# Optimization experiments

Hardware: AMD Instinct MI355X
Metric: run time of the kernel (lower is better)

The kernel has to match this reference:

```python
import jax, jax.numpy as jnp
from jax import lax
import numpy as np

B, T, F_IN, H = 64, 128, 12, 128  # batch, seq_len, input/output features, hidden


def _uinit(key, shape, fan):
    return jax.random.uniform(key, shape, jnp.float32, -1.0, 1.0) / np.float32(np.sqrt(fan))


def setup_inputs() -> dict:
    key = jax.random.key(0)
    ks = jax.random.split(key, 12)
    inp = {
        "x": jax.random.normal(ks[0], (B, T, F_IN), jnp.float32),
        # encoder LSTM (gate order i,f,g,o; b = b_ih + b_hh folded together)
        "enc_Wih": _uinit(ks[1], (4 * H, F_IN), H),
        "enc_Whh": _uinit(ks[2], (4 * H, H), H),
        "enc_b": _uinit(ks[3], (4 * H,), H),
        # decoder LSTM (input is the 12-dim teacher-forced x slice)
        "dec_Wih": _uinit(ks[4], (4 * H, F_IN), H),
        "dec_Whh": _uinit(ks[5], (4 * H, H), H),
        "dec_b": _uinit(ks[6], (4 * H,), H),
        # attention: Linear(2H -> H) with bias, then v: Linear(H -> 1, no bias)
        "attn_W": _uinit(ks[7], (H, 2 * H), 2 * H),
        "attn_b": _uinit(ks[8], (H,), 2 * H),
        "v_w": _uinit(ks[9], (H,), H),
        # output layer: Linear(2H -> F_IN)  (intended width; see notes)
        "out_W": _uinit(ks[10], (F_IN, 2 * H), 2 * H),
        "out_b": _uinit(ks[11], (F_IN,), 2 * H),
    }
    return inp


def _lstm_cell(xt, h, c, Wih, Whh, b):
    z = xt @ Wih.T + h @ Whh.T + b  # [B, 4H]
    i, f, g, o = jnp.split(z, 4, axis=-1)
    c = jax.nn.sigmoid(f) * c + jax.nn.sigmoid(i) * jnp.tanh(g)
    h = jax.nn.sigmoid(o) * jnp.tanh(c)
    return h, c


def reference(x, enc_Wih, enc_Whh, enc_b, dec_Wih, dec_Whh, dec_b,
              attn_W, attn_b, v_w, out_W, out_b):
    b_, t_, _ = x.shape
    hdim = enc_Whh.shape[1]
    xs = jnp.swapaxes(x, 0, 1)  # [T, B, F]
    h0 = jnp.zeros((b_, hdim), x.dtype)
    c0 = jnp.zeros((b_, hdim), x.dtype)

    def enc_step(carry, xt):
        h, c = carry
        h, c = _lstm_cell(xt, h, c, enc_Wih, enc_Whh, enc_b)
        return (h, c), h

    (hT, cT), enc_hs = lax.scan(enc_step, (h0, c0), xs)
    enc_out = jnp.swapaxes(enc_hs, 0, 1)  # [B, T, H]

    # split attn weight: cat(hidden, enc_out) @ W.T == hidden@W1.T + enc_out@W2.T
    W1, W2 = attn_W[:, :hdim], attn_W[:, hdim:]
    enc_proj = jnp.einsum("bth,gh->btg", enc_out, W2)  # precompute encoder side

    def dec_step(carry, xt):
        h, c = carry
        h, c = _lstm_cell(xt, h, c, dec_Wih, dec_Whh, dec_b)
        energy = jnp.tanh((h @ W1.T)[:, None, :] + enc_proj + attn_b)  # [B,T,H]
        score = jnp.einsum("bth,h->bt", energy, v_w)
        w = jax.nn.softmax(score, axis=1)  # attention over encoder time
        ctx = jnp.einsum("bt,bth->bh", w, enc_out)
        return (h, c), jnp.concatenate([h, ctx], axis=-1)  # [B, 2H]

    _, dec_ys = lax.scan(dec_step, (hT, cT), xs)
    dec_out = jnp.swapaxes(dec_ys, 0, 1)  # [B, T, 2H]
    return dec_out @ out_W.T + out_b  # [B, T, F]
```

## Files before the change

### kernel.cpp

```cpp
#include <hip/hip_runtime.h>
#include <hip/hip_bf16.h>

#define BB 64
#define TT 128
#define FIN 12
#define HH 128

#define LOG2E 1.4426950408889634f
#define TWO_LOG2E 2.8853900817779268f

__device__ __forceinline__ float fexp2(float x) { return __builtin_amdgcn_exp2f(x); }
__device__ __forceinline__ float frcp(float x)  { return __builtin_amdgcn_rcpf(x); }

__device__ __forceinline__ float tanh_f(float x) {
  return 1.0f - 2.0f * frcp(1.0f + fexp2(TWO_LOG2E * x));
}
__device__ __forceinline__ float sigm_f(float x) {
  return frcp(1.0f + fexp2(-LOG2E * x));
}

template <int CTRL>
__device__ __forceinline__ float dpp_addstage(float v) {
  int s = __builtin_amdgcn_update_dpp(0, __float_as_int(v), CTRL, 0xF, 0xF, true);
  return v + __int_as_float(s);
}
__device__ __forceinline__ float red8(float v) {
  v = dpp_addstage<0xB1>(v);
  v = dpp_addstage<0x4E>(v);
  v = dpp_addstage<0x141>(v);
  return v;
}

#define FMA4S(acc, s, v) do { \
  acc.x = fmaf((s), (v).x, acc.x); \
  acc.y = fmaf((s), (v).y, acc.y); \
  acc.z = fmaf((s), (v).z, acc.z); \
  acc.w = fmaf((s), (v).w, acc.w); } while (0)

#define ACC4(hv, wv, a) do { \
  a = fmaf((hv).x, (wv).x, a); a = fmaf((hv).y, (wv).y, a); \
  a = fmaf((hv).z, (wv).z, a); a = fmaf((hv).w, (wv).w, a); } while (0)

__device__ __forceinline__ void lstm_phase(
    const float* __restrict__ Wih, const float* __restrict__ Whh,
    const float* __restrict__ bias, float* __restrict__ Hout ,
    float* __restrict__ xs, float (*hbuf)[160], float* __restrict__ hist,
    const int tid, const int q, const int i, float& c)
{
  const int xo   = (q < 4) ? 3 * q : 0;
  const float xz = (q < 4) ? 1.0f : 0.0f;

  float4 wg[4][4];
  #pragma unroll
  for (int g = 0; g < 4; ++g)
    #pragma unroll
    for (int j = 0; j < 4; ++j)
      wg[g][j] = *(const float4*)(Whh + ((g * HH + i) * HH) + 16 * q + 4 * j);

  float wx[4][3];
  #pragma unroll
  for (int g = 0; g < 4; ++g)
    #pragma unroll
    for (int j = 0; j < 3; ++j)
      wx[g][j] = Wih[(g * HH + i) * FIN + xo + j] * xz;

  const float bi = bias[i], bf = bias[HH + i], bg = bias[2 * HH + i], bo = bias[3 * HH + i];

  int ts = 0;
  #pragma unroll 1
  for (int half = 0; half < 2; ++half) {
    #pragma unroll 1
    for (int tt = 0; tt < 64; ++tt, ++ts) {
      const int t = half * 64 + tt;
      __syncthreads();
      const float* hb = (const float*)hbuf[ts & 1] + q * 20;
      float4 h0 = *(const float4*)(hb + 0);
      float4 h1 = *(const float4*)(hb + 4);
      float4 h2 = *(const float4*)(hb + 8);
      float4 h3 = *(const float4*)(hb + 12);

      const float* xt = xs + t * FIN + xo;
      float x0 = xt[0], x1 = xt[1], x2 = xt[2];
      float ai = wx[0][0] * x0 + wx[0][1] * x1 + wx[0][2] * x2;
      float af = wx[1][0] * x0 + wx[1][1] * x1 + wx[1][2] * x2;
      float ag = wx[2][0] * x0 + wx[2][1] * x1 + wx[2][2] * x2;
      float ao = wx[3][0] * x0 + wx[3][1] * x1 + wx[3][2] * x2;

      ACC4(h0, wg[0][0], ai); ACC4(h0, wg[1][0], af); ACC4(h0, wg[2][0], ag); ACC4(h0, wg[3][0], ao);
      ACC4(h1, wg[0][1], ai); ACC4(h1, wg[1][1], af); ACC4(h1, wg[2][1], ag); ACC4(h1, wg[3][1], ao);
      ACC4(h2, wg[0][2], ai); ACC4(h2, wg[1][2], af); ACC4(h2, wg[2][2], ag); ACC4(h2, wg[3][2], ao);
      ACC4(h3, wg[0][3], ai); ACC4(h3, wg[1][3], af); ACC4(h3, wg[2][3], ag); ACC4(h3, wg[3][3], ao);

      ai = red8(ai); af = red8(af); ag = red8(ag); ao = red8(ao);

      if (q == 0) {
        float zi = sigm_f(ai + bi);
        float zf = sigm_f(af + bf);
        float zg = tanh_f(ag + bg);
        float zo = sigm_f(ao + bo);
        c = fmaf(zf, c, zi * zg);
        float hn = zo * tanh_f(c);
        hbuf[(ts + 1) & 1][(i >> 4) * 20 + (i & 15)] = hn;
        hist[tt * HH + i] = hn;
      }
    }
    __syncthreads();
    {
      float4* dst = (float4*)(Hout + (size_t)(half * 64) * HH);
      const float4* src = (const float4*)hist;
      dst[tid]        = src[tid];
      dst[tid + 1024] = src[tid + 1024];
    }
  }
}

__global__ __launch_bounds__(1024, 4) void lstm_enc_kernel(
    const float* __restrict__ x,
    const float* __restrict__ eWih, const float* __restrict__ eWhh, const float* __restrict__ eb,
    float* __restrict__ encH, float* __restrict__ decH)
{
  const int b   = blockIdx.x;
  const int tid = threadIdx.x;
  const int q   = tid & 7;
  const int i   = tid >> 3;

  __shared__ __align__(16) float xs[TT * FIN];
  __shared__ __align__(16) float hbuf[2][160];
  __shared__ __align__(16) float hist[64 * HH];

  if (tid < (TT * FIN / 4))
    ((float4*)xs)[tid] = ((const float4*)(x + (size_t)b * TT * FIN))[tid];
  if (tid < 320) ((float*)hbuf)[tid] = 0.0f;
  float c = 0.0f;

  lstm_phase(eWih, eWhh, eb, encH + (size_t)b * TT * HH, xs, hbuf, hist, tid, q, i, c);

  if (q == 0) decH[(size_t)b * TT * HH + i] = c;
}

__global__ __launch_bounds__(1024, 4) void lstm_dec_p_kernel(
    const float* __restrict__ x,
    const float* __restrict__ dWih, const float* __restrict__ dWhh, const float* __restrict__ db,
    const float* __restrict__ attnW, const float* __restrict__ outW,
    const float* __restrict__ encH,
    float* __restrict__ decH, float* __restrict__ Pbuf, float* __restrict__ y2buf)
{
  __shared__ __align__(16) float smem[12416];
  const int tid = threadIdx.x;

  if (blockIdx.x < 64) {
    const int b = blockIdx.x;
    const int q = tid & 7;
    const int i = tid >> 3;
    float* xs           = smem;
    float (*hbuf)[160]  = (float(*)[160])(smem + 1536);
    float* hist         = smem + 1856;

    if (tid < (TT * FIN / 4))
      ((float4*)xs)[tid] = ((const float4*)(x + (size_t)b * TT * FIN))[tid];
    if (tid < 128) {
      float hv = encH[((size_t)b * TT + 127) * HH + tid];
      hbuf[0][(tid >> 4) * 20 + (tid & 15)] = hv;
    }
    float c = 0.0f;
    if (q == 0) c = decH[(size_t)b * TT * HH + i];

    lstm_phase(dWih, dWhh, db, decH + (size_t)b * TT * HH, xs, hbuf, hist, tid, q, i, c);
  } else if (blockIdx.x < 192) {
    const int pb = blockIdx.x - 64;
    const int b  = pb & 63;
    const int r0 = (pb >> 6) * 64;
    float* WT = smem;
    float* Xt = smem + 4224;

    const float* X = encH + ((size_t)b * TT + r0) * HH;
    ((float4*)Xt)[tid]        = ((const float4*)X)[tid];
    ((float4*)Xt)[tid + 1024] = ((const float4*)X)[tid + 1024];

    const float* W = attnW + HH;
    const int hq = tid & 31, rr = tid >> 5;
    const int h0 = 4 * hq;

    float4 acc0 = make_float4(0.f, 0.f, 0.f, 0.f);
    float4 acc1 = acc0;

    #pragma unroll 1
    for (int kb = 0; kb < 4; ++kb) {
      __syncthreads();
      {
        int h = tid >> 3, koff = (tid & 7) * 4;
        float4 v = *(const float4*)(W + h * 256 + kb * 32 + koff);
        WT[(koff + 0) * 132 + h] = v.x;
        WT[(koff + 1) * 132 + h] = v.y;
        WT[(koff + 2) * 132 + h] = v.z;
        WT[(koff + 3) * 132 + h] = v.w;
      }
      __syncthreads();
      const float* xr0 = Xt + (2 * rr) * 128 + kb * 32;
      const float* xr1 = xr0 + 128;
      #pragma unroll
      for (int k4 = 0; k4 < 32; k4 += 4) {
        float4 xa = *(const float4*)(xr0 + k4);
        float4 xb = *(const float4*)(xr1 + k4);
        float4 w0 = *(const float4*)&WT[(k4 + 0) * 132 + h0];
        float4 w1 = *(const float4*)&WT[(k4 + 1) * 132 + h0];
        float4 w2 = *(const float4*)&WT[(k4 + 2) * 132 + h0];
        float4 w3 = *(const float4*)&WT[(k4 + 3) * 132 + h0];
        FMA4S(acc0, xa.x, w0); FMA4S(acc0, xa.y, w1);
        FMA4S(acc0, xa.z, w2); FMA4S(acc0, xa.w, w3);
        FMA4S(acc1, xb.x, w0); FMA4S(acc1, xb.y, w1);
        FMA4S(acc1, xb.z, w2); FMA4S(acc1, xb.w, w3);
      }
    }
    acc0.x = fexp2(TWO_LOG2E * acc0.x); acc0.y = fexp2(TWO_LOG2E * acc0.y);
    acc0.z = fexp2(TWO_LOG2E * acc0.z); acc0.w = fexp2(TWO_LOG2E * acc0.w);
    acc1.x = fexp2(TWO_LOG2E * acc1.x); acc1.y = fexp2(TWO_LOG2E * acc1.y);
    acc1.z = fexp2(TWO_LOG2E * acc1.z); acc1.w = fexp2(TWO_LOG2E * acc1.w);
    float* O = Pbuf + ((size_t)b * TT + r0) * HH;
    *(float4*)(O + (2 * rr) * 128 + h0)     = acc0;
    *(float4*)(O + (2 * rr + 1) * 128 + h0) = acc1;
  } else if (y2buf) {
    const int b = blockIdx.x - 192;
    float* w2l = smem;
    if (tid < 384) {
      int f = tid >> 5, k = (tid & 31) * 4;
      float4 wv = *(const float4*)(outW + f * 256 + 128 + k);
      *(float4*)&w2l[f * 132 + k] = wv;
    }
    __syncthreads();
    for (int j = tid; j < TT * 12; j += 1024) {
      int t = j / 12, f = j - 12 * t;
      const float* er = encH + ((size_t)b * TT + t) * HH;
      const float* wr = w2l + f * 132;
      float a = 0.f;
      #pragma unroll 8
      for (int k = 0; k < 32; ++k) {
        float4 ev = *(const float4*)(er + 4 * k);
        float4 wv = *(const float4*)(wr + 4 * k);
        ACC4(ev, wv, a);
      }
      y2buf[b * (TT * 16) + t * 16 + f] = a;
    }
  }
}

__global__ __launch_bounds__(256, 2) void projA_kernel(
    const float* __restrict__ decH, const float* __restrict__ attnW,
    const float* __restrict__ attnb, float* __restrict__ Abuf)
{
  const int b  = blockIdx.x & 63;
  const int r0 = (blockIdx.x >> 6) * 16;
  const int tid = threadIdx.x;

  __shared__ __align__(16) float WT[64 * 128];
  __shared__ __align__(16) float Xt[16 * 128];

  const float* X = decH + ((size_t)b * TT + r0) * HH;
  const float* W = attnW;

  ((float4*)Xt)[tid]       = ((const float4*)X)[tid];
  ((float4*)Xt)[256 + tid] = ((const float4*)X)[256 + tid];

  const int hq = tid & 31, rr = tid >> 5;
  const int h0 = 4 * hq;

  float4 acc0 = *(const float4*)(attnb + h0);
  float4 acc1 = acc0;

  for (int kb = 0; kb < 2; ++kb) {
    __syncthreads();
    {
      int h = tid >> 1, koff = (tid & 1) * 32;
      #pragma unroll
      for (int j = 0; j < 8; ++j) {
        float4 v = *(const float4*)(W + h * 256 + kb * 64 + koff + 4 * j);
        int kp = koff + 4 * j;
        WT[(kp + 0) * 128 + h] = v.x;
        WT[(kp + 1) * 128 + h] = v.y;
        WT[(kp + 2) * 128 + h] = v.z;
        WT[(kp + 3) * 128 + h] = v.w;
      }
    }
    __syncthreads();
    const float* xr0 = Xt + (2 * rr) * 128 + kb * 64;
    const float* xr1 = xr0 + 128;
    #pragma unroll
    for (int k4 = 0; k4 < 64; k4 += 4) {
      float4 xa = *(const float4*)(xr0 + k4);
      float4 xb = *(const float4*)(xr1 + k4);
      float4 w0 = *(const float4*)&WT[(k4 + 0) * 128 + h0];
      float4 w1 = *(const float4*)&WT[(k4 + 1) * 128 + h0];
      float4 w2 = *(const float4*)&WT[(k4 + 2) * 128 + h0];
      float4 w3 = *(const float4*)&WT[(k4 + 3) * 128 + h0];
      FMA4S(acc0, xa.x, w0); FMA4S(acc0, xa.y, w1);
      FMA4S(acc0, xa.z, w2); FMA4S(acc0, xa.w, w3);
      FMA4S(acc1, xb.x, w0); FMA4S(acc1, xb.y, w1);
      FMA4S(acc1, xb.z, w2); FMA4S(acc1, xb.w, w3);
    }
  }
  acc0.x = fexp2(TWO_LOG2E * acc0.x); acc0.y = fexp2(TWO_LOG2E * acc0.y);
  acc0.z = fexp2(TWO_LOG2E * acc0.z); acc0.w = fexp2(TWO_LOG2E * acc0.w);
  acc1.x = fexp2(TWO_LOG2E * acc1.x); acc1.y = fexp2(TWO_LOG2E * acc1.y);
  acc1.z = fexp2(TWO_LOG2E * acc1.z); acc1.w = fexp2(TWO_LOG2E * acc1.w);
  float* O = Abuf + ((size_t)b * TT + r0) * HH;
  *(float4*)(O + (2 * rr) * 128 + h0)     = acc0;
  *(float4*)(O + (2 * rr + 1) * 128 + h0) = acc1;
}

#define AST 132
#define Y2ST 20

template <bool HY2>
__global__ __launch_bounds__(512, 2) void attn_kernel(
    const float* __restrict__ encH, const float* __restrict__ decH,
    const float* __restrict__ Pbuf, const float* __restrict__ Abuf,
    const float* __restrict__ y2buf,
    const float* __restrict__ vw, const float* __restrict__ outW,
    const float* __restrict__ outb, float* __restrict__ out)
{
  const int b  = blockIdx.x >> 3;
  const int s0 = (blockIdx.x & 7) * 16;
  const int tid = threadIdx.x;

  __shared__ __align__(16) float buf[64 * 128];
  __shared__ __align__(16) float a_lds[16 * AST];
  __shared__ __align__(16) float sc[16 * AST];
  __shared__ __align__(16) float dh[16 * 128];
  __shared__ __align__(16) float vl[HH];
  __shared__ __align__(16) float y2s[TT * Y2ST];
  __shared__ __align__(16) float w2l[12 * AST];

  ((float4*)dh)[tid] = ((const float4*)(decH + ((size_t)b * TT + s0) * HH))[tid];
  if (tid < 32) ((float4*)vl)[tid] = ((const float4*)vw)[tid];
  {
    int r = tid >> 5, c4 = (tid & 31) * 4;
    float4 av = *(const float4*)(Abuf + ((size_t)b * TT + s0 + r) * HH + c4);
    *(float4*)&a_lds[r * AST + c4] = av;
  }
  if constexpr (HY2) {
    if (tid < 512) {
      float4 v = ((const float4*)(y2buf + (size_t)b * (TT * 16)))[tid];
      int t = tid >> 2, g = (tid & 3) * 4;
      *(float4*)&y2s[t * Y2ST + g] = v;
    }
  } else {
    if (tid < 384) {
      int f = tid >> 5, k = (tid & 31) * 4;
      float4 wv = *(const float4*)(outW + f * 256 + 128 + k);
      *(float4*)&w2l[f * AST + k] = wv;
    }
  }

  const int u  = tid & 31;
  const int sl = tid >> 5;
  const int uq = u & 15;
  const int uh = u >> 4;

  for (int half = 0; half < 2; ++half) {
    const int tbase = half * 64;
    __syncthreads();
    #pragma unroll
    for (int i = 0; i < 4; ++i) {
      int flat = i * 2048 + tid * 4;
      int tp = flat >> 7;
      int h0 = flat & 127;
      float4 v = *(const float4*)(Pbuf + ((size_t)b * TT + tbase + tp) * HH + h0);
      int tq = tp >> 2, tr = tp & 3;
      buf[(h0 + 0) * 64 + 4 * ((tq ^ ((h0 + 0) >> 2)) & 15) + tr] = v.x;
      buf[(h0 + 1) * 64 + 4 * ((tq ^ ((h0 + 1) >> 2)) & 15) + tr] = v.y;
      buf[(h0 + 2) * 64 + 4 * ((tq ^ ((h0 + 2) >> 2)) & 15) + tr] = v.z;
      buf[(h0 + 3) * 64 + 4 * ((tq ^ ((h0 + 3) >> 2)) & 15) + tr] = v.w;
    }
    __syncthreads();
    float4 acc = make_float4(0.f, 0.f, 0.f, 0.f);
    const float* earow = a_lds + sl * AST;
    #pragma unroll 4
    for (int hh = 0; hh < 64; hh += 4) {
      const int h = uh * 64 + hh;
      float4 ea = *(const float4*)&earow[h];
      float4 va = *(const float4*)&vl[h];
      const int xoff = 4 * ((uq ^ ((h >> 2) & 15)) & 15);
      float4 p0 = *(const float4*)&buf[(h + 0) * 64 + xoff];
      float4 p1 = *(const float4*)&buf[(h + 1) * 64 + xoff];
      float4 p2 = *(const float4*)&buf[(h + 2) * 64 + xoff];
      float4 p3 = *(const float4*)&buf[(h + 3) * 64 + xoff];
      acc.x = fmaf(va.x, frcp(fmaf(ea.x, p0.x, 1.f)), acc.x);
      acc.y = fmaf(va.x, frcp(fmaf(ea.x, p0.y, 1.f)), acc.y);
      acc.z = fmaf(va.x, frcp(fmaf(ea.x, p0.z, 1.f)), acc.z);
      acc.w = fmaf(va.x, frcp(fmaf(ea.x, p0.w, 1.f)), acc.w);
      acc.x = fmaf(va.y, frcp(fmaf(ea.y, p1.x, 1.f)), acc.x);
      acc.y = fmaf(va.y, frcp(fmaf(ea.y, p1.y, 1.f)), acc.y);
      acc.z = fmaf(va.y, frcp(fmaf(ea.y, p1.z, 1.f)), acc.z);
      acc.w = fmaf(va.y, frcp(fmaf(ea.y, p1.w, 1.f)), acc.w);
      acc.x = fmaf(va.z, frcp(fmaf(ea.z, p2.x, 1.f)), acc.x);
      acc.y = fmaf(va.z, frcp(fmaf(ea.z, p2.y, 1.f)), acc.y);
      acc.z = fmaf(va.z, frcp(fmaf(ea.z, p2.z, 1.f)), acc.z);
      acc.w = fmaf(va.z, frcp(fmaf(ea.z, p2.w, 1.f)), acc.w);
      acc.x = fmaf(va.w, frcp(fmaf(ea.w, p3.x, 1.f)), acc.x);
      acc.y = fmaf(va.w, frcp(fmaf(ea.w, p3.y, 1.f)), acc.y);
      acc.z = fmaf(va.w, frcp(fmaf(ea.w, p3.z, 1.f)), acc.z);
      acc.w = fmaf(va.w, frcp(fmaf(ea.w, p3.w, 1.f)), acc.w);
    }
    acc.x += __shfl_xor(acc.x, 16, 64);
    acc.y += __shfl_xor(acc.y, 16, 64);
    acc.z += __shfl_xor(acc.z, 16, 64);
    acc.w += __shfl_xor(acc.w, 16, 64);
    if (uh == 0) {
      float4 o;
      o.x = -2.f * acc.x; o.y = -2.f * acc.y;
      o.z = -2.f * acc.z; o.w = -2.f * acc.w;
      *(float4*)&sc[sl * AST + tbase + 4 * uq] = o;
    }
  }
  __syncthreads();

  {
    float4 sv = *(const float4*)&sc[sl * AST + 4 * u];
    float mx = fmaxf(fmaxf(sv.x, sv.y), fmaxf(sv.z, sv.w));
    #pragma unroll
    for (int msk = 1; msk <= 16; msk <<= 1) mx = fmaxf(mx, __shfl_xor(mx, msk, 64));
    float4 e;
    e.x = fexp2(LOG2E * (sv.x - mx));
    e.y = fexp2(LOG2E * (sv.y - mx));
    e.z = fexp2(LOG2E * (sv.z - mx));
    e.w = fexp2(LOG2E * (sv.w - mx));
    float sm = (e.x + e.y) + (e.z + e.w);
    #pragma unroll
    for (int msk = 1; msk <= 16; msk <<= 1) sm += __shfl_xor(sm, msk, 64);
    float r = frcp(sm);
    e.x *= r; e.y *= r; e.z *= r; e.w *= r;
    *(float4*)&sc[sl * AST + 4 * u] = e;
  }

  if constexpr (!HY2) {
    for (int half = 0; half < 2; ++half) {
      const int tbase = half * 64;
      __syncthreads();
      #pragma unroll
      for (int i = 0; i < 4; ++i) {
        int flat = i * 2048 + tid * 4;
        int tp = flat >> 7;
        int hh0 = flat & 127;
        *(float4*)&buf[tp * 128 + hh0] =
            *(const float4*)(encH + ((size_t)b * TT + tbase + tp) * HH + hh0);
      }
      __syncthreads();
      {
        int j = tid;
        int t = j / 12, f = j - 12 * t;
        float a = 0.f;
        const float* br = buf + t * 128;
        const float* wr = w2l + f * AST;
        #pragma unroll 8
        for (int k = 0; k < 32; ++k) {
          float4 bv = *(const float4*)(br + 4 * k);
          float4 wv = *(const float4*)(wr + 4 * k);
          ACC4(bv, wv, a);
        }
        y2s[(tbase + t) * Y2ST + f] = a;
        if (tid < 256) {
          int j2 = tid + 512;
          int t2 = j2 / 12, f2 = j2 - 12 * t2;
          float a2 = 0.f;
          const float* br2 = buf + t2 * 128;
          const float* wr2 = w2l + f2 * AST;
          #pragma unroll 8
          for (int k = 0; k < 32; ++k) {
            float4 bv = *(const float4*)(br2 + 4 * k);
            float4 wv = *(const float4*)(wr2 + 4 * k);
            ACC4(bv, wv, a2);
          }
          y2s[(tbase + t2) * Y2ST + f2] = a2;
        }
      }
    }
  }
  __syncthreads();

  if (tid < 192) {
    int s = tid / 12, f = tid - 12 * (tid / 12);
    float acc = outb[f];
    const float4* w4 = (const float4*)(outW + f * 256);
    const float4* d4 = (const float4*)(dh + s * 128);
    #pragma unroll
    for (int k = 0; k < 32; ++k) {
      float4 wv = w4[k], dv = d4[k];
      acc = fmaf(wv.x, dv.x, acc); acc = fmaf(wv.y, dv.y, acc);
      acc = fmaf(wv.z, dv.z, acc); acc = fmaf(wv.w, dv.w, acc);
    }
    const float* wrow = sc + s * AST;
    #pragma unroll 8
    for (int t = 0; t < TT; ++t)
      acc = fmaf(wrow[t], y2s[t * Y2ST + f], acc);
    out[((size_t)b * TT + s0 + s) * FIN + f] = acc;
  }
}

extern "C" void kernel_launch(void* const* d_in, const int* in_sizes, int n_in,
                              void* d_out, int out_size, void* d_ws, size_t ws_size,
                              hipStream_t stream)
{
  const float* x     = (const float*)d_in[0];
  const float* eWih  = (const float*)d_in[1];
  const float* eWhh  = (const float*)d_in[2];
  const float* eb    = (const float*)d_in[3];
  const float* dWih  = (const float*)d_in[4];
  const float* dWhh  = (const float*)d_in[5];
  const float* db    = (const float*)d_in[6];
  const float* attnW = (const float*)d_in[7];
  const float* attnb = (const float*)d_in[8];
  const float* vw    = (const float*)d_in[9];
  const float* outW  = (const float*)d_in[10];
  const float* outb  = (const float*)d_in[11];
  float* out = (float*)d_out;

  float* ws   = (float*)d_ws;
  const size_t SEG = (size_t)BB * TT * HH;
  float* encH = ws;
  float* decH = ws + SEG;
  float* Pbuf = ws + 2 * SEG;
  float* Abuf = ws + 3 * SEG;
  float* y2buf = ws + 4 * SEG;

  const size_t need_bytes = (4 * SEG + (size_t)BB * TT * 16) * sizeof(float);
  const bool have_y2 = ws_size >= need_bytes;

  lstm_enc_kernel<<<64, 1024, 0, stream>>>(x, eWih, eWhh, eb, encH, decH);
  if (have_y2) {
    lstm_dec_p_kernel<<<256, 1024, 0, stream>>>(x, dWih, dWhh, db, attnW, outW,
                                                encH, decH, Pbuf, y2buf);
    projA_kernel<<<512, 256, 0, stream>>>(decH, attnW, attnb, Abuf);
    attn_kernel<true><<<512, 512, 0, stream>>>(encH, decH, Pbuf, Abuf, y2buf,
                                               vw, outW, outb, out);
  } else {
    lstm_dec_p_kernel<<<192, 1024, 0, stream>>>(x, dWih, dWhh, db, attnW, outW,
                                                encH, decH, Pbuf, nullptr);
    projA_kernel<<<512, 256, 0, stream>>>(decH, attnW, attnb, Abuf);
    attn_kernel<false><<<512, 512, 0, stream>>>(encH, decH, Pbuf, Abuf, nullptr,
                                                vw, outW, outb, out);
  }
}
```

Measured before the change: 314.9 us.

## Fuse decoder attention projection into attention kernel and widen per-block query tile

The separate projA kernel is folded into the attention kernel, so the W1·h projection and its exp transform are computed in LDS and never round-trip through a global Abuf. Each block now handles 32 decoder steps instead of 16, which halves the number of blocks and amortizes the Pbuf transpose loads over more queries. The tanh-energy score is computed through a reciprocal identity on precomputed exponentials. In exchange, each block repeats the attnW load and transpose, LDS use per block grows, and only 256 blocks are launched, which reduces occupancy across the GPU.

```diff
diff --git a/kernel.cpp b/kernel.cpp
--- a/kernel.cpp
+++ b/kernel.cpp
@@ -310,11 +310,175 @@
 #define AST 132
 #define Y2ST 20
 
-template <bool HY2>
-__global__ __launch_bounds__(512, 2) void attn_kernel(
+__global__ __launch_bounds__(512, 2) void attn_fused_kernel(
+    const float* __restrict__ decH, const float* __restrict__ Pbuf,
+    const float* __restrict__ y2buf,
+    const float* __restrict__ attnW, const float* __restrict__ attnb,
+    const float* __restrict__ vw, const float* __restrict__ outW,
+    const float* __restrict__ outb, float* __restrict__ out)
+{
+  const int b  = blockIdx.x >> 2;
+  const int s0 = (blockIdx.x & 3) * 32;
+  const int tid = threadIdx.x;
+
+  __shared__ __align__(16) float buf[64 * 128];
+  __shared__ __align__(16) float a_lds[32 * AST];
+  __shared__ __align__(16) float sc[32 * AST];
+  __shared__ __align__(16) float dh[32 * 128];
+  __shared__ __align__(16) float vl[HH];
+  __shared__ __align__(16) float y2s[TT * Y2ST];
+
+  ((float4*)dh)[tid]       = ((const float4*)(decH + ((size_t)b * TT + s0) * HH))[tid];
+  ((float4*)dh)[tid + 512] = ((const float4*)(decH + ((size_t)b * TT + s0) * HH))[tid + 512];
+  if (tid < 32) ((float4*)vl)[tid] = ((const float4*)vw)[tid];
+  {
+    float4 v = ((const float4*)(y2buf + (size_t)b * (TT * 16)))[tid];
+    int t = tid >> 2, g = (tid & 3) * 4;
+    *(float4*)&y2s[t * Y2ST + g] = v;
+  }
+
+  const int hq = tid & 31, rr = tid >> 5;
+  const int h0 = 4 * hq;
+  {
+    float4 acc0 = *(const float4*)(attnb + h0);
+    float4 acc1 = acc0;
+    #pragma unroll 1
+    for (int kb = 0; kb < 2; ++kb) {
+      __syncthreads();
+      {
+        int h = tid >> 2, koff = (tid & 3) * 16;
+        #pragma unroll
+        for (int j = 0; j < 4; ++j) {
+          float4 v = *(const float4*)(attnW + h * 256 + kb * 64 + koff + 4 * j);
+          int kp = koff + 4 * j;
+          buf[(kp + 0) * 128 + h] = v.x;
+          buf[(kp + 1) * 128 + h] = v.y;
+          buf[(kp + 2) * 128 + h] = v.z;
+          buf[(kp + 3) * 128 + h] = v.w;
+        }
+      }
+      __syncthreads();
+      const float* xr0 = dh + (2 * rr) * 128 + kb * 64;
+      const float* xr1 = xr0 + 128;
+      #pragma unroll
+      for (int k4 = 0; k4 < 64; k4 += 4) {
+        float4 xa = *(const float4*)(xr0 + k4);
+        float4 xb = *(const float4*)(xr1 + k4);
+        float4 w0 = *(const float4*)&buf[(k4 + 0) * 128 + h0];
+        float4 w1 = *(const float4*)&buf[(k4 + 1) * 128 + h0];
+        float4 w2 = *(const float4*)&buf[(k4 + 2) * 128 + h0];
+        float4 w3 = *(const float4*)&buf[(k4 + 3) * 128 + h0];
+        FMA4S(acc0, xa.x, w0); FMA4S(acc0, xa.y, w1);
+        FMA4S(acc0, xa.z, w2); FMA4S(acc0, xa.w, w3);
+        FMA4S(acc1, xb.x, w0); FMA4S(acc1, xb.y, w1);
+        FMA4S(acc1, xb.z, w2); FMA4S(acc1, xb.w, w3);
+      }
+    }
+    acc0.x = fexp2(TWO_LOG2E * acc0.x); acc0.y = fexp2(TWO_LOG2E * acc0.y);
+    acc0.z = fexp2(TWO_LOG2E * acc0.z); acc0.w = fexp2(TWO_LOG2E * acc0.w);
+    acc1.x = fexp2(TWO_LOG2E * acc1.x); acc1.y = fexp2(TWO_LOG2E * acc1.y);
+    acc1.z = fexp2(TWO_LOG2E * acc1.z); acc1.w = fexp2(TWO_LOG2E * acc1.w);
+    *(float4*)&a_lds[(2 * rr) * AST + h0]     = acc0;
+    *(float4*)&a_lds[(2 * rr + 1) * AST + h0] = acc1;
+  }
+
+  const int uq = tid & 15;
+  const int sl = tid >> 4;
+
+  float4 sA, sB;
+  #pragma unroll 1
+  for (int half = 0; half < 2; ++half) {
+    __syncthreads();
+    #pragma unroll
+    for (int i = 0; i < 4; ++i) {
+      int flat = i * 2048 + tid * 4;
+      int tp = flat >> 7;
+      int hh0 = flat & 127;
+      float4 v = *(const float4*)(Pbuf + ((size_t)b * TT + half * 64 + tp) * HH + hh0);
+      int tq = tp >> 2, tr = tp & 3;
+      buf[(hh0 + 0) * 64 + 4 * ((tq ^ ((hh0 + 0) >> 2)) & 15) + tr] = v.x;
+      buf[(hh0 + 1) * 64 + 4 * ((tq ^ ((hh0 + 1) >> 2)) & 15) + tr] = v.y;
+      buf[(hh0 + 2) * 64 + 4 * ((tq ^ ((hh0 + 2) >> 2)) & 15) + tr] = v.z;
+      buf[(hh0 + 3) * 64 + 4 * ((tq ^ ((hh0 + 3) >> 2)) & 15) + tr] = v.w;
+    }
+    __syncthreads();
+    float4 acc = make_float4(0.f, 0.f, 0.f, 0.f);
+    const float* earow = a_lds + sl * AST;
+    #pragma unroll 4
+    for (int h = 0; h < 128; h += 4) {
+      float4 ea = *(const float4*)&earow[h];
+      float4 va = *(const float4*)&vl[h];
+      const int xoff = 4 * ((uq ^ ((h >> 2) & 15)) & 15);
+      float4 p0 = *(const float4*)&buf[(h + 0) * 64 + xoff];
+      float4 p1 = *(const float4*)&buf[(h + 1) * 64 + xoff];
+      float4 p2 = *(const float4*)&buf[(h + 2) * 64 + xoff];
+      float4 p3 = *(const float4*)&buf[(h + 3) * 64 + xoff];
+      acc.x = fmaf(va.x, frcp(fmaf(ea.x, p0.x, 1.f)), acc.x);
+      acc.y = fmaf(va.x, frcp(fmaf(ea.x, p0.y, 1.f)), acc.y);
+      acc.z = fmaf(va.x, frcp(fmaf(ea.x, p0.z, 1.f)), acc.z);
+      acc.w = fmaf(va.x, frcp(fmaf(ea.x, p0.w, 1.f)), acc.w);
+      acc.x = fmaf(va.y, frcp(fmaf(ea.y, p1.x, 1.f)), acc.x);
+      acc.y = fmaf(va.y, frcp(fmaf(ea.y, p1.y, 1.f)), acc.y);
+      acc.z = fmaf(va.y, frcp(fmaf(ea.y, p1.z, 1.f)), acc.z);
+      acc.w = fmaf(va.y, frcp(fmaf(ea.y, p1.w, 1.f)), acc.w);
+      acc.x = fmaf(va.z, frcp(fmaf(ea.z, p2.x, 1.f)), acc.x);
+      acc.y = fmaf(va.z, frcp(fmaf(ea.z, p2.y, 1.f)), acc.y);
+      acc.z = fmaf(va.z, frcp(fmaf(ea.z, p2.z, 1.f)), acc.z);
+      acc.w = fmaf(va.z, frcp(fmaf(ea.z, p2.w, 1.f)), acc.w);
+      acc.x = fmaf(va.w, frcp(fmaf(ea.w, p3.x, 1.f)), acc.x);
+      acc.y = fmaf(va.w, frcp(fmaf(ea.w, p3.y, 1.f)), acc.y);
+      acc.z = fmaf(va.w, frcp(fmaf(ea.w, p3.z, 1.f)), acc.z);
+      acc.w = fmaf(va.w, frcp(fmaf(ea.w, p3.w, 1.f)), acc.w);
+    }
+    float4 o;
+    o.x = -2.f * acc.x; o.y = -2.f * acc.y;
+    o.z = -2.f * acc.z; o.w = -2.f * acc.w;
+    if (half == 0) sA = o; else sB = o;
+  }
+
+  {
+    float mx = fmaxf(fmaxf(fmaxf(sA.x, sA.y), fmaxf(sA.z, sA.w)),
+                     fmaxf(fmaxf(sB.x, sB.y), fmaxf(sB.z, sB.w)));
+    #pragma unroll
+    for (int msk = 1; msk <= 8; msk <<= 1) mx = fmaxf(mx, __shfl_xor(mx, msk, 64));
+    float4 eA, eB;
+    eA.x = fexp2(LOG2E * (sA.x - mx)); eA.y = fexp2(LOG2E * (sA.y - mx));
+    eA.z = fexp2(LOG2E * (sA.z - mx)); eA.w = fexp2(LOG2E * (sA.w - mx));
+    eB.x = fexp2(LOG2E * (sB.x - mx)); eB.y = fexp2(LOG2E * (sB.y - mx));
+    eB.z = fexp2(LOG2E * (sB.z - mx)); eB.w = fexp2(LOG2E * (sB.w - mx));
+    float sm = ((eA.x + eA.y) + (eA.z + eA.w)) + ((eB.x + eB.y) + (eB.z + eB.w));
+    #pragma unroll
+    for (int msk = 1; msk <= 8; msk <<= 1) sm += __shfl_xor(sm, msk, 64);
+    float r = frcp(sm);
+    eA.x *= r; eA.y *= r; eA.z *= r; eA.w *= r;
+    eB.x *= r; eB.y *= r; eB.z *= r; eB.w *= r;
+    *(float4*)&sc[sl * AST + 4 * uq]      = eA;
+    *(float4*)&sc[sl * AST + 64 + 4 * uq] = eB;
+  }
+  __syncthreads();
+
+  if (tid < 384) {
+    int s = tid / 12, f = tid - 12 * (tid / 12);
+    float acc = outb[f];
+    const float4* w4 = (const float4*)(outW + f * 256);
+    const float4* d4 = (const float4*)(dh + s * 128);
+    #pragma unroll
+    for (int k = 0; k < 32; ++k) {
+      float4 wv = w4[k], dv = d4[k];
+      acc = fmaf(wv.x, dv.x, acc); acc = fmaf(wv.y, dv.y, acc);
+      acc = fmaf(wv.z, dv.z, acc); acc = fmaf(wv.w, dv.w, acc);
+    }
+    const float* wrow = sc + s * AST;
+    #pragma unroll 8
+    for (int t = 0; t < TT; ++t)
+      acc = fmaf(wrow[t], y2s[t * Y2ST + f], acc);
+    out[((size_t)b * TT + s0 + s) * FIN + f] = acc;
+  }
+}
+
+__global__ __launch_bounds__(512, 2) void attn_kernel_fb(
     const float* __restrict__ encH, const float* __restrict__ decH,
     const float* __restrict__ Pbuf, const float* __restrict__ Abuf,
-    const float* __restrict__ y2buf,
     const float* __restrict__ vw, const float* __restrict__ outW,
     const float* __restrict__ outb, float* __restrict__ out)
 {
@@ -337,18 +501,10 @@
     float4 av = *(const float4*)(Abuf + ((size_t)b * TT + s0 + r) * HH + c4);
     *(float4*)&a_lds[r * AST + c4] = av;
   }
-  if constexpr (HY2) {
-    if (tid < 512) {
-      float4 v = ((const float4*)(y2buf + (size_t)b * (TT * 16)))[tid];
-      int t = tid >> 2, g = (tid & 3) * 4;
-      *(float4*)&y2s[t * Y2ST + g] = v;
-    }
-  } else {
-    if (tid < 384) {
-      int f = tid >> 5, k = (tid & 31) * 4;
-      float4 wv = *(const float4*)(outW + f * 256 + 128 + k);
-      *(float4*)&w2l[f * AST + k] = wv;
-    }
+  if (tid < 384) {
+    int f = tid >> 5, k = (tid & 31) * 4;
+    float4 wv = *(const float4*)(outW + f * 256 + 128 + k);
+    *(float4*)&w2l[f * AST + k] = wv;
   }
 
   const int u  = tid & 31;
@@ -432,46 +588,44 @@
     *(float4*)&sc[sl * AST + 4 * u] = e;
   }
 
-  if constexpr (!HY2) {
-    for (int half = 0; half < 2; ++half) {
-      const int tbase = half * 64;
-      __syncthreads();
-      #pragma unroll
-      for (int i = 0; i < 4; ++i) {
-        int flat = i * 2048 + tid * 4;
-        int tp = flat >> 7;
-        int hh0 = flat & 127;
-        *(float4*)&buf[tp * 128 + hh0] =
-            *(const float4*)(encH + ((size_t)b * TT + tbase + tp) * HH + hh0);
-      }
-      __syncthreads();
-      {
-        int j = tid;
-        int t = j / 12, f = j - 12 * t;
-        float a = 0.f;
-        const float* br = buf + t * 128;
-        const float* wr = w2l + f * AST;
+  for (int half = 0; half < 2; ++half) {
+    const int tbase = half * 64;
+    __syncthreads();
+    #pragma unroll
+    for (int i = 0; i < 4; ++i) {
+      int flat = i * 2048 + tid * 4;
+      int tp = flat >> 7;
+      int hh0 = flat & 127;
+      *(float4*)&buf[tp * 128 + hh0] =
+          *(const float4*)(encH + ((size_t)b * TT + tbase + tp) * HH + hh0);
+    }
+    __syncthreads();
+    {
+      int j = tid;
+      int t = j / 12, f = j - 12 * t;
+      float a = 0.f;
+      const float* br = buf + t * 128;
+      const float* wr = w2l + f * AST;
+      #pragma unroll 8
+      for (int k = 0; k < 32; ++k) {
+        float4 bv = *(const float4*)(br + 4 * k);
+        float4 wv = *(const float4*)(wr + 4 * k);
+        ACC4(bv, wv, a);
+      }
+      y2s[(tbase + t) * Y2ST + f] = a;
+      if (tid < 256) {
+        int j2 = tid + 512;
+        int t2 = j2 / 12, f2 = j2 - 12 * t2;
+        float a2 = 0.f;
+        const float* br2 = buf + t2 * 128;
+        const float* wr2 = w2l + f2 * AST;
         #pragma unroll 8
         for (int k = 0; k < 32; ++k) {
-          float4 bv = *(const float4*)(br + 4 * k);
-          float4 wv = *(const float4*)(wr + 4 * k);
-          ACC4(bv, wv, a);
+          float4 bv = *(const float4*)(br2 + 4 * k);
+          float4 wv = *(const float4*)(wr2 + 4 * k);
+          ACC4(bv, wv, a2);
         }
-        y2s[(tbase + t) * Y2ST + f] = a;
-        if (tid < 256) {
-          int j2 = tid + 512;
-          int t2 = j2 / 12, f2 = j2 - 12 * t2;
-          float a2 = 0.f;
-          const float* br2 = buf + t2 * 128;
-          const float* wr2 = w2l + f2 * AST;
-          #pragma unroll 8
-          for (int k = 0; k < 32; ++k) {
-            float4 bv = *(const float4*)(br2 + 4 * k);
-            float4 wv = *(const float4*)(wr2 + 4 * k);
-            ACC4(bv, wv, a2);
-          }
-          y2s[(tbase + t2) * Y2ST + f2] = a2;
-        }
+        y2s[(tbase + t2) * Y2ST + f2] = a2;
       }
     }
   }
@@ -529,14 +683,13 @@
   if (have_y2) {
     lstm_dec_p_kernel<<<256, 1024, 0, stream>>>(x, dWih, dWhh, db, attnW, outW,
                                                 encH, decH, Pbuf, y2buf);
-    projA_kernel<<<512, 256, 0, stream>>>(decH, attnW, attnb, Abuf);
-    attn_kernel<true><<<512, 512, 0, stream>>>(encH, decH, Pbuf, Abuf, y2buf,
+    attn_fused_kernel<<<256, 512, 0, stream>>>(decH, Pbuf, y2buf, attnW, attnb,
                                                vw, outW, outb, out);
   } else {
     lstm_dec_p_kernel<<<192, 1024, 0, stream>>>(x, dWih, dWhh, db, attnW, outW,
                                                 encH, decH, Pbuf, nullptr);
     projA_kernel<<<512, 256, 0, stream>>>(decH, attnW, attnb, Abuf);
-    attn_kernel<false><<<512, 512, 0, stream>>>(encH, decH, Pbuf, Abuf, nullptr,
-                                                vw, outW, outb, out);
-  }
-}
+    attn_kernel_fb<<<512, 512, 0, stream>>>(encH, decH, Pbuf, Abuf,
+                                            vw, outW, outb, out);
+  }
+}
```

Result: no change. 315.2 us (+0.1%).
